# Kernel tuning notes

Hardware: AMD Instinct MI355X
Metric: run time of the kernel (lower is better)

## Reference

```python
import jax, jax.numpy as jnp
import numpy as np

DEGREES = [1, 2, 3]
SEG_IDS = np.repeat(np.arange(len(DEGREES)), [2 * l + 1 for l in DEGREES])  # (m_tot,)
M_TOT = int(SEG_IDS.shape[0])  # 15
N_NODES, F, F_IN, N_TYPE = 24576, 512, 512, 10


def setup_inputs() -> dict:
    key = jax.random.key(0)
    ks = jax.random.split(key, 8)
    s = 1.0 / np.sqrt(F).astype(np.float32)
    return {
        "x": jax.random.normal(ks[0], (N_NODES, F_IN), jnp.float32),
        "chi": jax.random.normal(ks[1], (N_NODES, M_TOT), jnp.float32),
        "z_one_hot": jax.nn.one_hot(jax.random.randint(ks[2], (N_NODES,), 0, N_TYPE), N_TYPE, dtype=jnp.float32),
        "W1": jax.random.normal(ks[3], (F_IN, F), jnp.float32) * s,
        "b1": jnp.zeros((F,), jnp.float32),
        "W2": jax.random.normal(ks[4], (F, F), jnp.float32) * s,
        "W3": jax.random.normal(ks[5], (F, 1), jnp.float32) * s,
        "W4": jax.random.normal(ks[6], (len(DEGREES) * F, F_IN), jnp.float32) * (1.0 / np.sqrt(len(DEGREES) * F).astype(np.float32)),
        "b4": jnp.zeros((F_IN,), jnp.float32),
    }


def _l0_contraction(x_chi):
    # make_l0_contraction_fn(degrees), vmapped over the feature axis:
    # per degree l, sum over its (2l+1) m-components of x_chi**2.
    # x_chi: (n, m_tot, F) -> (n, n_degrees, F)
    sq = jnp.swapaxes(x_chi * x_chi, 0, 1)  # (m_tot, n, F)
    out = jax.ops.segment_sum(sq, jnp.asarray(SEG_IDS), num_segments=len(DEGREES))
    return jnp.swapaxes(out, 0, 1)


def reference(x, chi, z_one_hot, W1, b1, W2, W3, W4, b4):
    # max_body_order == 2 -> SymmetricContraction branch is skipped (x_chi_bo = x_chi)
    h = x @ W1 + b1                              # Dense(features)(x): (n, F)
    x_chi = h[:, None, :] * chi[:, :, None]      # (n, m_tot, F)
    x_chi = x_chi @ W2                           # Dense(features, use_bias=False): (n, m_tot, F)
    chi_bo = (x_chi @ W3)[..., 0]                # Dense(1, use_bias=False).squeeze(-1): (n, m_tot)
    inv = _l0_contraction(x_chi).reshape(x.shape[0], -1)  # (n, n_degrees*F)
    x_bo = jax.nn.silu(inv @ W4 + b4)            # Dense(x.shape[-1]): (n, F_in)
    return (x_bo, chi_bo)
```

## Files before the change

kernel.cpp:

```cpp
#include <hip/hip_runtime.h>

typedef __bf16 bf16_t;
typedef __bf16 bf16x8 __attribute__((ext_vector_type(8)));
typedef float f32x4 __attribute__((ext_vector_type(4)));

#define BK 64
#define NNODES 24576


__device__ __forceinline__ void g2l16(const void* g, void* l) {
    __builtin_amdgcn_global_load_lds((__attribute__((address_space(1))) void*)(g),
                                     (__attribute__((address_space(3))) void*)(l),
                                     16, 0, 0);
}

#define SB()  __builtin_amdgcn_sched_barrier(0)
#define BAR() __builtin_amdgcn_s_barrier()

__global__ __launch_bounds__(1024)
void gemm16_kernel(const bf16_t* __restrict__ A, const bf16_t* __restrict__ Bt,
                   const float* __restrict__ bias, void* __restrict__ Cout,
                   int N, int K, int mode,
                   const float* __restrict__ W3, const float* __restrict__ c3v,
                   float* __restrict__ sbuf)
{
    __shared__ __align__(16) bf16_t lA[2][12288];
    __shared__ __align__(16) bf16_t lB[2][16384];

    const int tid  = threadIdx.x;
    const int lane = tid & 63;
    const int wave = tid >> 6;
    const int wr   = wave >> 2;
    const int wc   = wave & 3;
    const int l15  = lane & 15;
    const int lh   = lane >> 4;

    const int bm = blockIdx.x;
    const int bn = blockIdx.y;

    const size_t strb = (size_t)K * 2;

    const int q0 = tid * 16;
    const size_t ro = (size_t)(q0 >> 7) * strb + ((q0 ^ (((q0 >> 7) & 7) << 4)) & 127);
    const char* gA = (const char*)A  + (size_t)bm * 192 * strb + ro;
    const char* gB = (const char*)Bt + (size_t)bn * 256 * strb + ro;
    char* baseA = (char*)&lA[0][0];
    char* baseB = (char*)&lB[0][0];

    auto stage = [&](int t, int buf) {
        const size_t kb = (size_t)t * 128;
        g2l16(gA + kb, baseA + buf * 24576 + q0);
        if (tid < 512)
            g2l16(gA + kb + 128 * strb, baseA + buf * 24576 + 16384 + q0);
        g2l16(gB + kb, baseB + buf * 32768 + q0);
        g2l16(gB + kb + 128 * strb, baseB + buf * 32768 + 16384 + q0);
    };

    const int swzr = (l15 & 7) << 4;
    const int xk0  = (lh * 16) ^ swzr;
    const int xk1  = (64 + lh * 16) ^ swzr;
    const int aOff = (wr * 48 + l15) * 128;
    const int bOff = (wc * 64 + l15) * 128;

    f32x4 acc[3][4] = {};

    const int T = K / BK;
    stage(0, 0);

    for (int t = 0; t < T; ++t) {
        const int buf = t & 1;

        asm volatile("s_waitcnt vmcnt(0)" ::: "memory");
        BAR();
        SB();

        if (t + 1 < T) stage(t + 1, buf ^ 1);
        SB();

        bf16x8 af[3][2], bf[4][2];
        {
            const char* _pa = baseA + buf * 24576 + aOff;
#pragma unroll
            for (int m = 0; m < 3; ++m) {
                af[m][0] = *(const bf16x8*)(_pa + m * 2048 + xk0);
                af[m][1] = *(const bf16x8*)(_pa + m * 2048 + xk1);
            }
            const char* _pb = baseB + buf * 32768 + bOff;
#pragma unroll
            for (int n = 0; n < 4; ++n) {
                bf[n][0] = *(const bf16x8*)(_pb + n * 2048 + xk0);
                bf[n][1] = *(const bf16x8*)(_pb + n * 2048 + xk1);
            }
        }

        __builtin_amdgcn_s_setprio(1);
#pragma unroll
        for (int m = 0; m < 3; ++m)
#pragma unroll
        for (int n = 0; n < 4; ++n)
#pragma unroll
        for (int kk = 0; kk < 2; ++kk)
            acc[m][n] = __builtin_amdgcn_mfma_f32_16x16x32_bf16(
                af[m][kk], bf[n][kk], acc[m][n], 0, 0, 0);
        __builtin_amdgcn_s_setprio(0);
    }

    const int gr0 = bm * 192 + wr * 48 + lh * 4;
    const int gc0 = bn * 256 + wc * 64 + l15;
    if (mode == 0) {
        bf16_t* C = (bf16_t*)Cout;
#pragma unroll
        for (int m = 0; m < 3; ++m)
#pragma unroll
        for (int n = 0; n < 4; ++n) {
            const int c = gc0 + n * 16;
            const float bv = bias ? bias[c] : 0.f;
#pragma unroll
            for (int j = 0; j < 4; ++j)
                C[(size_t)(gr0 + m * 16 + j) * N + c] = (bf16_t)(acc[m][n][j] + bv);
        }
    } else if (mode == 1) {
        float* C = (float*)Cout;
#pragma unroll
        for (int m = 0; m < 3; ++m)
#pragma unroll
        for (int n = 0; n < 4; ++n) {
            const int c = gc0 + n * 16;
            const float bv = bias[c];
#pragma unroll
            for (int j = 0; j < 4; ++j) {
                float v = acc[m][n][j] + bv;
                C[(size_t)(gr0 + m * 16 + j) * N + c] = v / (1.f + __expf(-v));
            }
        }
    } else {
        bf16_t* A3 = (bf16_t*)Cout;
        float w3v[4], bv[4];
#pragma unroll
        for (int n = 0; n < 4; ++n) {
            w3v[n] = W3[gc0 + n * 16];
            bv[n]  = bias[gc0 + n * 16];
        }
#pragma unroll
        for (int m = 0; m < 3; ++m)
#pragma unroll
        for (int j = 0; j < 4; ++j) {
            const int r = gr0 + m * 16 + j;
            float g[4], p = 0.f;
#pragma unroll
            for (int n = 0; n < 4; ++n) {
                g[n] = acc[m][n][j] + bv[n];
                p += g[n] * w3v[n];
            }
            p += __shfl_xor(p, 1); p += __shfl_xor(p, 2);
            p += __shfl_xor(p, 4); p += __shfl_xor(p, 8);
            if (l15 == 0) atomicAdd(&sbuf[r], p);
            const float c0 = c3v[r], c1 = c3v[r + NNODES], c2 = c3v[r + 2 * NNODES];
            bf16_t* arow = A3 + (size_t)r * 1536 + gc0;
#pragma unroll
            for (int n = 0; n < 4; ++n) {
                const float g2 = g[n] * g[n];
                arow[n * 16]        = (bf16_t)(c0 * g2);
                arow[n * 16 + 512]  = (bf16_t)(c1 * g2);
                arow[n * 16 + 1024] = (bf16_t)(c2 * g2);
            }
        }
    }
}

__global__ __launch_bounds__(512)
void gemm8_kernel(const bf16_t* __restrict__ A, const bf16_t* __restrict__ Bt,
                  void* __restrict__ Cout, int N, int K, int LD)
{
    __shared__ __align__(16) bf16_t lA[2][16384];
    __shared__ __align__(16) bf16_t lB[2][16384];

    const int tid  = threadIdx.x;
    const int lane = tid & 63;
    const int wave = tid >> 6;
    const int wr   = wave >> 2;
    const int wc   = wave & 3;
    const int l15  = lane & 15;
    const int lh   = lane >> 4;

    const int bm = blockIdx.x;
    const int bn = blockIdx.y;
    const int bz = blockIdx.z;

    const size_t strb = (size_t)LD * 2;
    const size_t zoff = (size_t)bz * K * 2;

    const int q0 = tid * 16;
    const size_t rowOff = (size_t)(q0 >> 7) * strb + ((q0 ^ (((q0 >> 7) & 7) << 4)) & 127);
    const char* gA = (const char*)A  + (size_t)bm * 256 * strb + zoff + rowOff;
    const char* gB = (const char*)Bt + (size_t)bn * 256 * strb + zoff + rowOff;
    char* baseA = (char*)&lA[0][0];
    char* baseB = (char*)&lB[0][0];

    auto stageA = [&](int t, int buf, int r) {
        g2l16(gA + (size_t)t * 128 + (size_t)(r * 64) * strb,
              baseA + buf * 32768 + r * 8192 + q0);
    };
    auto stageB = [&](int t, int buf, int r) {
        g2l16(gB + (size_t)t * 128 + (size_t)(r * 64) * strb,
              baseB + buf * 32768 + r * 8192 + q0);
    };

    const int swzr = (l15 & 7) << 4;
    const int xk0  = (lh * 16) ^ swzr;
    const int xk1  = (64 + lh * 16) ^ swzr;
    const int aOff = wr * 16384 + l15 * 128;
    const int bOff = wc * 8192 + l15 * 128;

    f32x4 acc[2][2][4][2] = {};

    const int T = K / BK;

#pragma unroll
    for (int r = 0; r < 4; ++r) { stageA(0, 0, r); stageB(0, 0, r); }

    for (int t = 0; t < T; ++t) {
        const int buf = t & 1, nbuf = buf ^ 1;

        asm volatile("s_waitcnt vmcnt(0)" ::: "memory");
        BAR();
        SB();

        if (t + 1 < T) {
#pragma unroll
            for (int r = 0; r < 4; ++r) { stageA(t + 1, nbuf, r); stageB(t + 1, nbuf, r); }
        }
        SB();

        bf16x8 af[8][2], bf[4][2];
        {
            const char* _pa = baseA + buf * 32768 + aOff;
#pragma unroll
            for (int i = 0; i < 8; ++i) {
                af[i][0] = *(const bf16x8*)(_pa + i * 2048 + xk0);
                af[i][1] = *(const bf16x8*)(_pa + i * 2048 + xk1);
            }
            const char* _pb = baseB + buf * 32768 + bOff;
#pragma unroll
            for (int j = 0; j < 4; ++j) {
                bf[j][0] = *(const bf16x8*)(_pb + j * 2048 + xk0);
                bf[j][1] = *(const bf16x8*)(_pb + j * 2048 + xk1);
            }
        }

        __builtin_amdgcn_s_setprio(1);
#pragma unroll
        for (int mh = 0; mh < 2; ++mh)
#pragma unroll
        for (int nh = 0; nh < 2; ++nh)
#pragma unroll
        for (int m = 0; m < 4; ++m)
#pragma unroll
        for (int n = 0; n < 2; ++n)
#pragma unroll
        for (int kk = 0; kk < 2; ++kk)
            acc[mh][nh][m][n] = __builtin_amdgcn_mfma_f32_16x16x32_bf16(
                af[mh * 4 + m][kk], bf[nh * 2 + n][kk], acc[mh][nh][m][n], 0, 0, 0);
        __builtin_amdgcn_s_setprio(0);
    }

    float* C = (float*)Cout + (size_t)bz * 512 * 512;
    const int gr0 = bm * 256 + wr * 128 + lh * 4;
    const int gc0 = bn * 256 + wc * 64 + l15;
#pragma unroll
    for (int mh = 0; mh < 2; ++mh)
#pragma unroll
    for (int nh = 0; nh < 2; ++nh)
#pragma unroll
    for (int m = 0; m < 4; ++m)
#pragma unroll
    for (int n = 0; n < 2; ++n) {
        const int c = gc0 + nh * 32 + n * 16;
#pragma unroll
        for (int j = 0; j < 4; ++j)
            C[(size_t)(gr0 + (mh * 4 + m) * 16 + j) * N + c] = acc[mh][nh][m][n][j];
    }
}

__global__ void wct_reduce_kernel(const float* __restrict__ p, bf16_t* __restrict__ out) {
    const int i = blockIdx.x * 256 + threadIdx.x;
    out[i] = (bf16_t)(p[i] + p[i + 262144] + p[i + 524288] + p[i + 786432]);
}

__global__ void cast8_kernel(const float* __restrict__ in, bf16_t* __restrict__ out, int n8) {
    const int i = blockIdx.x * blockDim.x + threadIdx.x;
    if (i >= n8) return;
    const float4* pp = (const float4*)in + (size_t)i * 2;
    float4 a = pp[0], b = pp[1];
    bf16x8 v;
    v[0] = (bf16_t)a.x; v[1] = (bf16_t)a.y; v[2] = (bf16_t)a.z; v[3] = (bf16_t)a.w;
    v[4] = (bf16_t)b.x; v[5] = (bf16_t)b.y; v[6] = (bf16_t)b.z; v[7] = (bf16_t)b.w;
    *(bf16x8*)(out + (size_t)i * 8) = v;
}

__global__ void prep_kernel(const float* __restrict__ W1, bf16_t* __restrict__ W1b,
                            const float* __restrict__ W2, bf16_t* __restrict__ W2t,
                            const float* __restrict__ W4, bf16_t* __restrict__ W4t)
{
    const int b = blockIdx.x;
    if (b < 128) {
        const int i = b * 256 + threadIdx.x;
        const float4* p = (const float4*)W1 + (size_t)i * 2;
        float4 a = p[0], c = p[1];
        bf16x8 v;
        v[0] = (bf16_t)a.x; v[1] = (bf16_t)a.y; v[2] = (bf16_t)a.z; v[3] = (bf16_t)a.w;
        v[4] = (bf16_t)c.x; v[5] = (bf16_t)c.y; v[6] = (bf16_t)c.z; v[7] = (bf16_t)c.w;
        *(bf16x8*)(W1b + (size_t)i * 8) = v;
    } else if (b < 1152) {
        const int idx = (b - 128) * 256 + threadIdx.x;
        const int c = idx >> 9, r = idx & 511;
        W2t[idx] = (bf16_t)W2[(size_t)r * 512 + c];
    } else {
        const int idx = (b - 1152) * 256 + threadIdx.x;
        const int c = idx / 1536, r = idx - c * 1536;
        W4t[idx] = (bf16_t)W4[(size_t)r * 512 + c];
    }
}

__global__ void vecmat_kernel(const float* __restrict__ v, const float* __restrict__ W,
                              float* __restrict__ out) {
    const int t = blockIdx.x * blockDim.x + threadIdx.x;
    if (t >= 512) return;
    float s = 0.f;
    for (int i = 0; i < 512; ++i) s += v[i] * W[i * 512 + t];
    out[t] = s;
}

__global__ void c3_kernel(const float* __restrict__ chi, float* __restrict__ c3) {
    const int n = blockIdx.x * 256 + threadIdx.x;
    if (n >= NNODES) return;
    const float* ch = chi + (size_t)n * 15;
    float a = 0.f, b = 0.f, c = 0.f;
#pragma unroll
    for (int m = 0; m < 3; ++m)  a += ch[m] * ch[m];
#pragma unroll
    for (int m = 3; m < 8; ++m)  b += ch[m] * ch[m];
#pragma unroll
    for (int m = 8; m < 15; ++m) c += ch[m] * ch[m];
    c3[n] = a; c3[n + NNODES] = b; c3[n + 2 * NNODES] = c;
}

__global__ void chbo_kernel(const float* __restrict__ chi, const float* __restrict__ s,
                            float* __restrict__ chbo) {
    const int idx = blockIdx.x * 256 + threadIdx.x;
    if (idx >= NNODES * 15) return;
    chbo[idx] = chi[idx] * s[idx / 15];
}

extern "C" void kernel_launch(void* const* d_in, const int* in_sizes, int n_in,
                              void* d_out, int out_size, void* d_ws, size_t ws_size,
                              hipStream_t stream)
{
    const float* x   = (const float*)d_in[0];
    const float* chi = (const float*)d_in[1];
    const float* W1  = (const float*)d_in[3];
    const float* b1  = (const float*)d_in[4];
    const float* W2  = (const float*)d_in[5];
    const float* W3  = (const float*)d_in[6];
    const float* W4  = (const float*)d_in[7];
    const float* b4  = (const float*)d_in[8];

    char* ws = (char*)d_ws;
    bf16_t* W1b  = (bf16_t*)(ws + 0);
    bf16_t* W2t  = (bf16_t*)(ws + 524288);
    bf16_t* W4t  = (bf16_t*)(ws + 1048576);
    bf16_t* Wct  = (bf16_t*)(ws + 2621440);
    float*  bc   = (float*) (ws + 3145728);
    float*  u    = (float*) (ws + 3147776);
    bf16_t* A3   = (bf16_t*)(ws + 3149824);
    float*  Wctp = (float*) (ws + 3149824);

    float*  xbo  = (float*)d_out;
    float*  chbo = (float*)d_out + (size_t)NNODES * 512;
    char*   c0s  = (char*)d_out;
    bf16_t* Xb   = (bf16_t*)(c0s + 0);
    float*  c3   = (float*) (c0s + 25165824);
    float*  sbuf = (float*) (c0s + 25460736);

    cast8_kernel<<<6144, 256, 0, stream>>>(x, Xb, 1572864);
    prep_kernel<<<4224, 256, 0, stream>>>(W1, W1b, W2, W2t, W4, W4t);
    vecmat_kernel<<<2, 256, 0, stream>>>(b1, W1, u);
    vecmat_kernel<<<2, 256, 0, stream>>>(u, W2, bc);
    c3_kernel<<<96, 256, 0, stream>>>(chi, c3);
    hipMemsetAsync(sbuf, 0, NNODES * sizeof(float), stream);

    gemm8_kernel<<<dim3(2, 2, 4), 512, 0, stream>>>(W2t, W1b, Wctp, 512, 128, 512);
    wct_reduce_kernel<<<1024, 256, 0, stream>>>(Wctp, Wct);

    gemm16_kernel<<<dim3(128, 2), 1024, 0, stream>>>(
        Xb, Wct, bc, A3, 512, 512, 3, W3, c3, sbuf);

    chbo_kernel<<<1440, 256, 0, stream>>>(chi, sbuf, chbo);

    gemm16_kernel<<<dim3(128, 2), 1024, 0, stream>>>(
        A3, W4t, b4, xbo, 512, 1536, 1, nullptr, nullptr, nullptr);
}
```

Measured before the change: 164.3 us.

## Factor per-degree chi scale out of A3 and apply it inside final GEMM

```diff
diff --git a/kernel.cpp b/kernel.cpp
--- a/kernel.cpp
+++ b/kernel.cpp
@@ -21,8 +21,7 @@
 void gemm16_kernel(const bf16_t* __restrict__ A, const bf16_t* __restrict__ Bt,
                    const float* __restrict__ bias, void* __restrict__ Cout,
                    int N, int K, int mode,
-                   const float* __restrict__ W3, const float* __restrict__ c3v,
-                   float* __restrict__ sbuf)
+                   const float* __restrict__ W3, float* __restrict__ sbuf)
 {
     __shared__ __align__(16) bf16_t lA[2][12288];
     __shared__ __align__(16) bf16_t lB[2][16384];
@@ -134,7 +133,7 @@
             }
         }
     } else {
-        bf16_t* A3 = (bf16_t*)Cout;
+        bf16_t* G2 = (bf16_t*)Cout;
         float w3v[4], bv[4];
 #pragma unroll
         for (int n = 0; n < 4; ++n) {
@@ -155,15 +154,141 @@
             p += __shfl_xor(p, 1); p += __shfl_xor(p, 2);
             p += __shfl_xor(p, 4); p += __shfl_xor(p, 8);
             if (l15 == 0) atomicAdd(&sbuf[r], p);
-            const float c0 = c3v[r], c1 = c3v[r + NNODES], c2 = c3v[r + 2 * NNODES];
-            bf16_t* arow = A3 + (size_t)r * 1536 + gc0;
+            bf16_t* grow = G2 + (size_t)r * 512 + gc0;
+#pragma unroll
+            for (int n = 0; n < 4; ++n)
+                grow[n * 16] = (bf16_t)(g[n] * g[n]);
+        }
+    }
+}
+
+__global__ __launch_bounds__(1024)
+void gemm16f_kernel(const bf16_t* __restrict__ G2, const bf16_t* __restrict__ W4t,
+                    const float* __restrict__ b4, const float* __restrict__ c3v,
+                    float* __restrict__ xbo)
+{
+    __shared__ __align__(16) bf16_t lA[2][12288];
+    __shared__ __align__(16) bf16_t lB[2][16384];
+
+    const int tid  = threadIdx.x;
+    const int lane = tid & 63;
+    const int wave = tid >> 6;
+    const int wr   = wave >> 2;
+    const int wc   = wave & 3;
+    const int l15  = lane & 15;
+    const int lh   = lane >> 4;
+
+    const int bm = blockIdx.x;
+    const int bn = blockIdx.y;
+
+    const size_t strbA = 1024;
+    const size_t strbB = 3072;
+
+    const int q0 = tid * 16;
+    const int qx = (q0 ^ (((q0 >> 7) & 7) << 4)) & 127;
+    const size_t roA = (size_t)(q0 >> 7) * strbA + qx;
+    const size_t roB = (size_t)(q0 >> 7) * strbB + qx;
+    const char* gA = (const char*)G2  + (size_t)bm * 192 * strbA + roA;
+    const char* gB = (const char*)W4t + (size_t)bn * 256 * strbB + roB;
+    char* baseA = (char*)&lA[0][0];
+    char* baseB = (char*)&lB[0][0];
+
+    auto stage = [&](int tt, int buf) {
+        const size_t kbA = (size_t)(tt & 7) * 128;
+        const size_t kbB = (size_t)tt * 128;
+        g2l16(gA + kbA, baseA + buf * 24576 + q0);
+        if (tid < 512)
+            g2l16(gA + kbA + 128 * strbA, baseA + buf * 24576 + 16384 + q0);
+        g2l16(gB + kbB, baseB + buf * 32768 + q0);
+        g2l16(gB + kbB + 128 * strbB, baseB + buf * 32768 + 16384 + q0);
+    };
+
+    const int swzr = (l15 & 7) << 4;
+    const int xk0  = (lh * 16) ^ swzr;
+    const int xk1  = (64 + lh * 16) ^ swzr;
+    const int aOff = (wr * 48 + l15) * 128;
+    const int bOff = (wc * 64 + l15) * 128;
+
+    const int gr0 = bm * 192 + wr * 48 + lh * 4;
+    const int gc0 = bn * 256 + wc * 64 + l15;
+
+    f32x4 acc[3][4] = {};
+
+    stage(0, 0);
+
+    for (int tt = 0; tt < 24; ++tt) {
+        const int buf = tt & 1;
+
+        asm volatile("s_waitcnt vmcnt(0)" ::: "memory");
+        BAR();
+        SB();
+
+        if (tt + 1 < 24) stage(tt + 1, buf ^ 1);
+        SB();
+
+        bf16x8 af[3][2], bf[4][2];
+        {
+            const char* _pa = baseA + buf * 24576 + aOff;
+#pragma unroll
+            for (int m = 0; m < 3; ++m) {
+                af[m][0] = *(const bf16x8*)(_pa + m * 2048 + xk0);
+                af[m][1] = *(const bf16x8*)(_pa + m * 2048 + xk1);
+            }
+            const char* _pb = baseB + buf * 32768 + bOff;
 #pragma unroll
             for (int n = 0; n < 4; ++n) {
-                const float g2 = g[n] * g[n];
-                arow[n * 16]        = (bf16_t)(c0 * g2);
-                arow[n * 16 + 512]  = (bf16_t)(c1 * g2);
-                arow[n * 16 + 1024] = (bf16_t)(c2 * g2);
-            }
+                bf[n][0] = *(const bf16x8*)(_pb + n * 2048 + xk0);
+                bf[n][1] = *(const bf16x8*)(_pb + n * 2048 + xk1);
+            }
+        }
+
+        __builtin_amdgcn_s_setprio(1);
+#pragma unroll
+        for (int m = 0; m < 3; ++m)
+#pragma unroll
+        for (int n = 0; n < 4; ++n)
+#pragma unroll
+        for (int kk = 0; kk < 2; ++kk)
+            acc[m][n] = __builtin_amdgcn_mfma_f32_16x16x32_bf16(
+                af[m][kk], bf[n][kk], acc[m][n], 0, 0, 0);
+        __builtin_amdgcn_s_setprio(0);
+
+        if (tt == 7) {
+#pragma unroll
+            for (int m = 0; m < 3; ++m)
+#pragma unroll
+            for (int j = 0; j < 4; ++j) {
+                const int r = gr0 + m * 16 + j;
+                const float ra = c3v[r] / fmaxf(c3v[r + NNODES], 1e-30f);
+#pragma unroll
+                for (int n = 0; n < 4; ++n) acc[m][n][j] *= ra;
+            }
+        } else if (tt == 15) {
+#pragma unroll
+            for (int m = 0; m < 3; ++m)
+#pragma unroll
+            for (int j = 0; j < 4; ++j) {
+                const int r = gr0 + m * 16 + j;
+                const float ra = fmaxf(c3v[r + NNODES], 1e-30f)
+                               / fmaxf(c3v[r + 2 * NNODES], 1e-30f);
+#pragma unroll
+                for (int n = 0; n < 4; ++n) acc[m][n][j] *= ra;
+            }
+        }
+    }
+
+#pragma unroll
+    for (int m = 0; m < 3; ++m)
+#pragma unroll
+    for (int j = 0; j < 4; ++j) {
+        const int r = gr0 + m * 16 + j;
+        const float c2 = fmaxf(c3v[r + 2 * NNODES], 1e-30f);
+        float* xrow = xbo + (size_t)r * 512;
+#pragma unroll
+        for (int n = 0; n < 4; ++n) {
+            const int c = gc0 + n * 16;
+            float v = acc[m][n][j] * c2 + b4[c];
+            xrow[c] = v / (1.f + __expf(-v));
         }
     }
 }
@@ -372,15 +497,14 @@
     bf16_t* Wct  = (bf16_t*)(ws + 2621440);
     float*  bc   = (float*) (ws + 3145728);
     float*  u    = (float*) (ws + 3147776);
-    bf16_t* A3   = (bf16_t*)(ws + 3149824);
-    float*  Wctp = (float*) (ws + 3149824);
+    float*  c3   = (float*) (ws + 3149824);
+    float*  sbuf = (float*) (ws + 3444736);
+    bf16_t* G2   = (bf16_t*)(ws + 3543040);
+    float*  Wctp = (float*) (ws + 3543040);
 
     float*  xbo  = (float*)d_out;
     float*  chbo = (float*)d_out + (size_t)NNODES * 512;
-    char*   c0s  = (char*)d_out;
-    bf16_t* Xb   = (bf16_t*)(c0s + 0);
-    float*  c3   = (float*) (c0s + 25165824);
-    float*  sbuf = (float*) (c0s + 25460736);
+    bf16_t* Xb   = (bf16_t*)d_out;
 
     cast8_kernel<<<6144, 256, 0, stream>>>(x, Xb, 1572864);
     prep_kernel<<<4224, 256, 0, stream>>>(W1, W1b, W2, W2t, W4, W4t);
@@ -393,10 +517,9 @@
     wct_reduce_kernel<<<1024, 256, 0, stream>>>(Wctp, Wct);
 
     gemm16_kernel<<<dim3(128, 2), 1024, 0, stream>>>(
-        Xb, Wct, bc, A3, 512, 512, 3, W3, c3, sbuf);
+        Xb, Wct, bc, G2, 512, 512, 3, W3, sbuf);
 
     chbo_kernel<<<1440, 256, 0, stream>>>(chi, sbuf, chbo);
 
-    gemm16_kernel<<<dim3(128, 2), 1024, 0, stream>>>(
-        A3, W4t, b4, xbo, 512, 1536, 1, nullptr, nullptr, nullptr);
-}
+    gemm16f_kernel<<<dim3(128, 2), 1024, 0, stream>>>(G2, W4t, b4, c3, xbo);
+}
```

Result: slower. 175.9 us (+7.1%).

## Fuse fp32-to-bf16 cast of x into first GEMM and drop sbuf memset

Applied to the files above, without the earlier changes.

```diff
diff --git a/kernel.cpp b/kernel.cpp
--- a/kernel.cpp
+++ b/kernel.cpp
@@ -2,6 +2,7 @@
 
 typedef __bf16 bf16_t;
 typedef __bf16 bf16x8 __attribute__((ext_vector_type(8)));
+typedef __bf16 bf16x4 __attribute__((ext_vector_type(4)));
 typedef float f32x4 __attribute__((ext_vector_type(4)));
 
 #define BK 64
@@ -18,11 +19,156 @@
 #define BAR() __builtin_amdgcn_s_barrier()
 
 __global__ __launch_bounds__(1024)
+void gemm16x_kernel(const float* __restrict__ X, const bf16_t* __restrict__ Bt,
+                    const float* __restrict__ bias, bf16_t* __restrict__ A3,
+                    const float* __restrict__ W3, const float* __restrict__ c3v,
+                    float* __restrict__ sbuf)
+{
+    __shared__ __align__(16) bf16_t lA[2][12288];
+    __shared__ __align__(16) bf16_t lB[2][16384];
+
+    const int tid  = threadIdx.x;
+    const int lane = tid & 63;
+    const int wave = tid >> 6;
+    const int wr   = wave >> 2;
+    const int wc   = wave & 3;
+    const int l15  = lane & 15;
+    const int lh   = lane >> 4;
+
+    const int bm = blockIdx.x;
+    const int bn = blockIdx.y;
+
+    const size_t strbB = 1024;
+
+    const int q0 = tid * 16;
+    const size_t roB = (size_t)(q0 >> 7) * strbB + ((q0 ^ (((q0 >> 7) & 7) << 4)) & 127);
+    const char* gB = (const char*)Bt + (size_t)bn * 256 * strbB + roB;
+    char* baseA = (char*)&lA[0][0];
+    char* baseB = (char*)&lB[0][0];
+
+    auto stageB = [&](int t, int buf) {
+        const size_t kb = (size_t)t * 128;
+        g2l16(gB + kb,                baseB + buf * 32768 + q0);
+        g2l16(gB + kb + 128 * strbB,  baseB + buf * 32768 + 16384 + q0);
+    };
+
+    const int arow0 = tid >> 4;
+    const int e4    = (tid & 15) * 4;
+    const float* gx = X + (size_t)(bm * 192 + arow0) * 512 + e4;
+    const int woff0 = ((arow0 * 128) + e4 * 2) ^ ((arow0 & 7) << 4);
+
+    float4 fA[3];
+    auto loadA = [&](int t) {
+#pragma unroll
+        for (int r = 0; r < 3; ++r)
+            fA[r] = *(const float4*)(gx + (size_t)r * 64 * 512 + t * 64);
+    };
+    auto writeA = [&](int buf) {
+        char* d = baseA + buf * 24576;
+#pragma unroll
+        for (int r = 0; r < 3; ++r) {
+            bf16x4 o;
+            o[0] = (bf16_t)fA[r].x; o[1] = (bf16_t)fA[r].y;
+            o[2] = (bf16_t)fA[r].z; o[3] = (bf16_t)fA[r].w;
+            *(bf16x4*)(d + r * 8192 + woff0) = o;
+        }
+    };
+
+    const int swzr = (l15 & 7) << 4;
+    const int xk0  = (lh * 16) ^ swzr;
+    const int xk1  = (64 + lh * 16) ^ swzr;
+    const int aOff = (wr * 48 + l15) * 128;
+    const int bOff = (wc * 64 + l15) * 128;
+
+    f32x4 acc[3][4] = {};
+
+    loadA(0); stageB(0, 0);
+    asm volatile("s_waitcnt vmcnt(2)" ::: "memory");
+    writeA(0);
+
+    for (int t = 0; t < 8; ++t) {
+        const int buf = t & 1;
+
+        asm volatile("s_waitcnt vmcnt(0) lgkmcnt(0)" ::: "memory");
+        BAR();
+        SB();
+
+        if (t < 7) { loadA(t + 1); stageB(t + 1, buf ^ 1); }
+        SB();
+
+        bf16x8 af[3][2], bf[4][2];
+        {
+            const char* _pa = baseA + buf * 24576 + aOff;
+#pragma unroll
+            for (int m = 0; m < 3; ++m) {
+                af[m][0] = *(const bf16x8*)(_pa + m * 2048 + xk0);
+                af[m][1] = *(const bf16x8*)(_pa + m * 2048 + xk1);
+            }
+            const char* _pb = baseB + buf * 32768 + bOff;
+#pragma unroll
+            for (int n = 0; n < 4; ++n) {
+                bf[n][0] = *(const bf16x8*)(_pb + n * 2048 + xk0);
+                bf[n][1] = *(const bf16x8*)(_pb + n * 2048 + xk1);
+            }
+        }
+
+        __builtin_amdgcn_s_setprio(1);
+#pragma unroll
+        for (int m = 0; m < 3; ++m)
+#pragma unroll
+        for (int n = 0; n < 4; ++n)
+#pragma unroll
+        for (int kk = 0; kk < 2; ++kk)
+            acc[m][n] = __builtin_amdgcn_mfma_f32_16x16x32_bf16(
+                af[m][kk], bf[n][kk], acc[m][n], 0, 0, 0);
+        __builtin_amdgcn_s_setprio(0);
+
+        if (t < 7) {
+            asm volatile("s_waitcnt vmcnt(2)" ::: "memory");
+            SB();
+            writeA(buf ^ 1);
+        }
+        SB();
+    }
+
+    const int gr0 = bm * 192 + wr * 48 + lh * 4;
+    const int gc0 = bn * 256 + wc * 64 + l15;
+    float w3v[4], bv[4];
+#pragma unroll
+    for (int n = 0; n < 4; ++n) {
+        w3v[n] = W3[gc0 + n * 16];
+        bv[n]  = bias[gc0 + n * 16];
+    }
+#pragma unroll
+    for (int m = 0; m < 3; ++m)
+#pragma unroll
+    for (int j = 0; j < 4; ++j) {
+        const int r = gr0 + m * 16 + j;
+        float g[4], p = 0.f;
+#pragma unroll
+        for (int n = 0; n < 4; ++n) {
+            g[n] = acc[m][n][j] + bv[n];
+            p += g[n] * w3v[n];
+        }
+        p += __shfl_xor(p, 1); p += __shfl_xor(p, 2);
+        p += __shfl_xor(p, 4); p += __shfl_xor(p, 8);
+        if (l15 == 0) atomicAdd(&sbuf[r], p);
+        const float c0 = c3v[r], c1 = c3v[r + NNODES], c2 = c3v[r + 2 * NNODES];
+        bf16_t* arow = A3 + (size_t)r * 1536 + gc0;
+#pragma unroll
+        for (int n = 0; n < 4; ++n) {
+            const float g2 = g[n] * g[n];
+            arow[n * 16]        = (bf16_t)(c0 * g2);
+            arow[n * 16 + 512]  = (bf16_t)(c1 * g2);
+            arow[n * 16 + 1024] = (bf16_t)(c2 * g2);
+        }
+    }
+}
+
+__global__ __launch_bounds__(1024)
 void gemm16_kernel(const bf16_t* __restrict__ A, const bf16_t* __restrict__ Bt,
                    const float* __restrict__ bias, void* __restrict__ Cout,
-                   int N, int K, int mode,
-                   const float* __restrict__ W3, const float* __restrict__ c3v,
-                   float* __restrict__ sbuf)
+                   int N, int K, int mode)
 {
     __shared__ __align__(16) bf16_t lA[2][12288];
     __shared__ __align__(16) bf16_t lB[2][16384];
@@ -119,7 +265,7 @@
             for (int j = 0; j < 4; ++j)
                 C[(size_t)(gr0 + m * 16 + j) * N + c] = (bf16_t)(acc[m][n][j] + bv);
         }
-    } else if (mode == 1) {
+    } else {
         float* C = (float*)Cout;
 #pragma unroll
         for (int m = 0; m < 3; ++m)
@@ -131,38 +277,6 @@
             for (int j = 0; j < 4; ++j) {
                 float v = acc[m][n][j] + bv;
                 C[(size_t)(gr0 + m * 16 + j) * N + c] = v / (1.f + __expf(-v));
-            }
-        }
-    } else {
-        bf16_t* A3 = (bf16_t*)Cout;
-        float w3v[4], bv[4];
-#pragma unroll
-        for (int n = 0; n < 4; ++n) {
-            w3v[n] = W3[gc0 + n * 16];
-            bv[n]  = bias[gc0 + n * 16];
-        }
-#pragma unroll
-        for (int m = 0; m < 3; ++m)
-#pragma unroll
-        for (int j = 0; j < 4; ++j) {
-            const int r = gr0 + m * 16 + j;
-            float g[4], p = 0.f;
-#pragma unroll
-            for (int n = 0; n < 4; ++n) {
-                g[n] = acc[m][n][j] + bv[n];
-                p += g[n] * w3v[n];
-            }
-            p += __shfl_xor(p, 1); p += __shfl_xor(p, 2);
-            p += __shfl_xor(p, 4); p += __shfl_xor(p, 8);
-            if (l15 == 0) atomicAdd(&sbuf[r], p);
-            const float c0 = c3v[r], c1 = c3v[r + NNODES], c2 = c3v[r + 2 * NNODES];
-            bf16_t* arow = A3 + (size_t)r * 1536 + gc0;
-#pragma unroll
-            for (int n = 0; n < 4; ++n) {
-                const float g2 = g[n] * g[n];
-                arow[n * 16]        = (bf16_t)(c0 * g2);
-                arow[n * 16 + 512]  = (bf16_t)(c1 * g2);
-                arow[n * 16 + 1024] = (bf16_t)(c2 * g2);
             }
         }
     }
@@ -285,17 +399,6 @@
 __global__ void wct_reduce_kernel(const float* __restrict__ p, bf16_t* __restrict__ out) {
     const int i = blockIdx.x * 256 + threadIdx.x;
     out[i] = (bf16_t)(p[i] + p[i + 262144] + p[i + 524288] + p[i + 786432]);
-}
-
-__global__ void cast8_kernel(const float* __restrict__ in, bf16_t* __restrict__ out, int n8) {
-    const int i = blockIdx.x * blockDim.x + threadIdx.x;
-    if (i >= n8) return;
-    const float4* pp = (const float4*)in + (size_t)i * 2;
-    float4 a = pp[0], b = pp[1];
-    bf16x8 v;
-    v[0] = (bf16_t)a.x; v[1] = (bf16_t)a.y; v[2] = (bf16_t)a.z; v[3] = (bf16_t)a.w;
-    v[4] = (bf16_t)b.x; v[5] = (bf16_t)b.y; v[6] = (bf16_t)b.z; v[7] = (bf16_t)b.w;
-    *(bf16x8*)(out + (size_t)i * 8) = v;
 }
 
 __global__ void prep_kernel(const float* __restrict__ W1, bf16_t* __restrict__ W1b,
@@ -331,7 +434,8 @@
     out[t] = s;
 }
 
-__global__ void c3_kernel(const float* __restrict__ chi, float* __restrict__ c3) {
+__global__ void c3_kernel(const float* __restrict__ chi, float* __restrict__ c3,
+                          float* __restrict__ sbuf) {
     const int n = blockIdx.x * 256 + threadIdx.x;
     if (n >= NNODES) return;
     const float* ch = chi + (size_t)n * 15;
@@ -343,6 +447,7 @@
 #pragma unroll
     for (int m = 8; m < 15; ++m) c += ch[m] * ch[m];
     c3[n] = a; c3[n + NNODES] = b; c3[n + 2 * NNODES] = c;
+    sbuf[n] = 0.f;
 }
 
 __global__ void chbo_kernel(const float* __restrict__ chi, const float* __restrict__ s,
@@ -378,25 +483,20 @@
     float*  xbo  = (float*)d_out;
     float*  chbo = (float*)d_out + (size_t)NNODES * 512;
     char*   c0s  = (char*)d_out;
-    bf16_t* Xb   = (bf16_t*)(c0s + 0);
     float*  c3   = (float*) (c0s + 25165824);
     float*  sbuf = (float*) (c0s + 25460736);
 
-    cast8_kernel<<<6144, 256, 0, stream>>>(x, Xb, 1572864);
     prep_kernel<<<4224, 256, 0, stream>>>(W1, W1b, W2, W2t, W4, W4t);
     vecmat_kernel<<<2, 256, 0, stream>>>(b1, W1, u);
     vecmat_kernel<<<2, 256, 0, stream>>>(u, W2, bc);
-    c3_kernel<<<96, 256, 0, stream>>>(chi, c3);
-    hipMemsetAsync(sbuf, 0, NNODES * sizeof(float), stream);
+    c3_kernel<<<96, 256, 0, stream>>>(chi, c3, sbuf);
 
     gemm8_kernel<<<dim3(2, 2, 4), 512, 0, stream>>>(W2t, W1b, Wctp, 512, 128, 512);
     wct_reduce_kernel<<<1024, 256, 0, stream>>>(Wctp, Wct);
 
-    gemm16_kernel<<<dim3(128, 2), 1024, 0, stream>>>(
-        Xb, Wct, bc, A3, 512, 512, 3, W3, c3, sbuf);
+    gemm16x_kernel<<<dim3(128, 2), 1024, 0, stream>>>(x, Wct, bc, A3, W3, c3, sbuf);
 
     chbo_kernel<<<1440, 256, 0, stream>>>(chi, sbuf, chbo);
 
-    gemm16_kernel<<<dim3(128, 2), 1024, 0, stream>>>(
-        A3, W4t, b4, xbo, 512, 1536, 1, nullptr, nullptr, nullptr);
-}
+    gemm16_kernel<<<dim3(128, 2), 1024, 0, stream>>>(A3, W4t, b4, xbo, 512, 1536, 1);
+}
```

Measured after the change: 159.8 us. 2.7% less time.
